# Kernel tuning notes

Measured on AMD Instinct MI355X. Metric: run time of the kernel, lower is better.

The kernel has to match this reference:

```python
import jax, jax.numpy as jnp
import numpy as np

LN_EPS = 1e-5

def _layernorm(x, g, b):
    mu = jnp.mean(x, axis=-1, keepdims=True)
    var = jnp.var(x, axis=-1, keepdims=True)
    return (x - mu) * jax.lax.rsqrt(var + LN_EPS) * g + b

def _attention(q_in, ctx, wq, wk, wv, wo, bo, n_heads):
    b, n, _ = q_in.shape
    m = ctx.shape[1]
    d_attn = wq.shape[1]
    d_head = d_attn // n_heads
    Q = (q_in @ wq).reshape(b, n, n_heads, d_head)
    K = (ctx @ wk).reshape(b, m, n_heads, d_head)
    V = (ctx @ wv).reshape(b, m, n_heads, d_head)
    scale = 1.0 / np.sqrt(d_head).astype(np.float32)
    sim = jnp.einsum('bnhd,bmhd->bhnm', Q, K) * scale
    attn = jax.nn.softmax(sim, axis=-1)
    out = jnp.einsum('bhnm,bmhd->bnhd', attn, V).reshape(b, n, d_attn)
    return out @ wo + bo

def setup_inputs() -> dict:
    key = jax.random.key(0)
    ks = jax.random.split(key, 16)
    B, N, D = 8, 1024, 640
    M, CD = 77, 768
    H = 4 * D  # GEGLU hidden = 2560
    s = lambda d: 1.0 / np.sqrt(d)
    return {
        'x': jax.random.normal(ks[0], (B, N, D), jnp.float32),
        'context': jax.random.normal(ks[1], (B, M, CD), jnp.float32),
        'sa_wq': jax.random.normal(ks[2], (D, D), jnp.float32) * s(D),
        'sa_wk': jax.random.normal(ks[3], (D, D), jnp.float32) * s(D),
        'sa_wv': jax.random.normal(ks[4], (D, D), jnp.float32) * s(D),
        'sa_wo': jax.random.normal(ks[5], (D, D), jnp.float32) * s(D),
        'sa_bo': jnp.zeros((D,), jnp.float32),
        'ca_wq': jax.random.normal(ks[6], (D, D), jnp.float32) * s(D),
        'ca_wk': jax.random.normal(ks[7], (CD, D), jnp.float32) * s(CD),
        'ca_wv': jax.random.normal(ks[8], (CD, D), jnp.float32) * s(CD),
        'ca_wo': jax.random.normal(ks[9], (D, D), jnp.float32) * s(D),
        'ca_bo': jnp.zeros((D,), jnp.float32),
        'ff_w1': jax.random.normal(ks[10], (D, 2 * H), jnp.float32) * s(D),
        'ff_b1': jnp.zeros((2 * H,), jnp.float32),
        'ff_w2': jax.random.normal(ks[11], (H, D), jnp.float32) * s(H),
        'ff_b2': jnp.zeros((D,), jnp.float32),
        'ln1_g': jnp.ones((D,), jnp.float32), 'ln1_b': jnp.zeros((D,), jnp.float32),
        'ln2_g': jnp.ones((D,), jnp.float32), 'ln2_b': jnp.zeros((D,), jnp.float32),
        'ln3_g': jnp.ones((D,), jnp.float32), 'ln3_b': jnp.zeros((D,), jnp.float32),
    }

def reference(x, context, sa_wq, sa_wk, sa_wv, sa_wo, sa_bo,
              ca_wq, ca_wk, ca_wv, ca_wo, ca_bo,
              ff_w1, ff_b1, ff_w2, ff_b2,
              ln1_g, ln1_b, ln2_g, ln2_b, ln3_g, ln3_b):
    n_heads = 8
    # post-norm residual block, matching norm_i(x + sublayer(x))
    x = _layernorm(x + _attention(x, x, sa_wq, sa_wk, sa_wv, sa_wo, sa_bo, n_heads), ln1_g, ln1_b)
    x = _layernorm(x + _attention(x, context, ca_wq, ca_wk, ca_wv, ca_wo, ca_bo, n_heads), ln2_g, ln2_b)
    h = x @ ff_w1 + ff_b1
    a, gate = jnp.split(h, 2, axis=-1)
    ff = (a * jax.nn.gelu(gate, approximate=False)) @ ff_w2 + ff_b2
    x = _layernorm(x + ff, ln3_g, ln3_b)
    return x
```

## Files before the change

### kernel.cpp

```cpp
#include <hip/hip_runtime.h>


using u16 = unsigned short;
typedef __attribute__((ext_vector_type(8))) short bfrag;
typedef __attribute__((ext_vector_type(4))) float f4;
typedef __attribute__((ext_vector_type(4))) unsigned short us4;

#define MFMA(a, b, c) __builtin_amdgcn_mfma_f32_16x16x32_bf16((a), (b), (c), 0, 0, 0)

__device__ __forceinline__ void gload16(const void* g, void* l) {
    __builtin_amdgcn_global_load_lds(
        (const __attribute__((address_space(1))) void*)g,
        (__attribute__((address_space(3))) void*)l, 16, 0, 0);
}

__device__ __forceinline__ u16 f2b(float f) {
    unsigned u = __float_as_uint(f);
    unsigned r = u + 0x7FFFu + ((u >> 16) & 1u);
    return (u16)(r >> 16);
}
__device__ __forceinline__ float b2f(u16 u) {
    return __uint_as_float(((unsigned)u) << 16);
}
__device__ __forceinline__ unsigned pack2(float a, float b) {
    return (unsigned)f2b(a) | ((unsigned)f2b(b) << 16);
}
__device__ __forceinline__ bfrag bzero() {
    bfrag z = {0,0,0,0,0,0,0,0};
    return z;
}
__device__ __forceinline__ float gelu_f(float x) {
    float y = 0.7978845608028654f * (x + 0.044715f * x * x * x);
    float e = exp2f(y * 2.8853900817779268f);
    float t = 1.0f - 2.0f * __builtin_amdgcn_rcpf(e + 1.0f);
    return 0.5f * x * (1.0f + t);
}

__device__ __forceinline__ void transp_tile(const float* __restrict__ in,
                                            u16* __restrict__ out,
                                            int K, int N, int ldo,
                                            int tile, bool perm,
                                            float (*t)[33])
{
    int nw = N >> 5;
    int n0 = (tile % nw) * 32, k0 = (tile / nw) * 32;
    int tx = threadIdx.x & 31, ty = threadIdx.x >> 5;
    #pragma unroll
    for (int i = 0; i < 32; i += 8)
        t[ty + i][tx] = in[(size_t)(k0 + ty + i) * N + n0 + tx];
    __syncthreads();
    #pragma unroll
    for (int i = 0; i < 32; i += 8) {
        int n = n0 + ty + i;
        int dst;
        if (perm) {
            dst = (n < 2560) ? ((n >> 5) * 64 + (n & 31))
                             : (((n - 2560) >> 5) * 64 + 32 + ((n - 2560) & 31));
        } else {
            dst = n;
        }
        out[(size_t)dst * ldo + k0 + tx] = f2b(t[tx][ty + i]);
    }
}

__global__ __launch_bounds__(256) void prep_k(
    const float* __restrict__ x, const float* __restrict__ ctx,
    const float* __restrict__ sa_wq, const float* __restrict__ sa_wk,
    const float* __restrict__ sa_wv, const float* __restrict__ sa_wo,
    const float* __restrict__ ca_wq, const float* __restrict__ ca_wk,
    const float* __restrict__ ca_wv, const float* __restrict__ ca_wo,
    const float* __restrict__ ff_w1, const float* __restrict__ ff_w2,
    u16* saqkvt, u16* sawot, u16* cawqt, u16* cawot, u16* cakvt,
    u16* ffw1t, u16* ffw2t, u16* xb, u16* ctxb)
{
    __shared__ float t[32][33];
    int b = blockIdx.x;
    if (b < 2400) {
        int task = b / 400, tile = b - task * 400;
        const float* src;
        u16* dst;
        if      (task == 0) { src = sa_wq; dst = saqkvt; }
        else if (task == 1) { src = sa_wk; dst = saqkvt + 409600; }
        else if (task == 2) { src = sa_wv; dst = saqkvt + 819200; }
        else if (task == 3) { src = sa_wo; dst = sawot; }
        else if (task == 4) { src = ca_wq; dst = cawqt; }
        else                { src = ca_wo; dst = cawot; }
        transp_tile(src, dst, 640, 640, 640, tile, false, t);
    } else if (b < 3360) {
        int tt = b - 2400;
        int task = tt / 480, tile = tt - task * 480;
        transp_tile(task ? ca_wv : ca_wk, cakvt + task * 491520, 768, 640, 768,
                    tile, false, t);
    } else if (b < 6560) {
        transp_tile(ff_w1, ffw1t, 640, 5120, 640, b - 3360, true, t);
    } else if (b < 8160) {
        transp_tile(ff_w2, ffw2t, 2560, 640, 2560, b - 6560, false, t);
    } else if (b < 10720) {
        int i = (b - 8160) * 256 + threadIdx.x;
        const float4* p = (const float4*)x + (size_t)i * 2;
        float4 a = p[0], bb = p[1];
        uint4 w = { pack2(a.x, a.y), pack2(a.z, a.w),
                    pack2(bb.x, bb.y), pack2(bb.z, bb.w) };
        ((uint4*)xb)[i] = w;
    } else {
        int i = (b - 10720) * 256 + threadIdx.x;
        int rowOut = i / 96, c8 = (i - rowOut * 96) * 8;
        int bb = rowOut / 80, r = rowOut - bb * 80;
        uint4 w = {0, 0, 0, 0};
        if (r < 77) {
            const float4* p = (const float4*)(ctx + ((size_t)(bb * 77 + r)) * 768 + c8);
            float4 a = p[0], b2 = p[1];
            w = (uint4){ pack2(a.x, a.y), pack2(a.z, a.w),
                         pack2(b2.x, b2.y), pack2(b2.z, b2.w) };
        }
        ((uint4*)ctxb)[i] = w;
    }
}

template<int MODE>
__device__ __forceinline__ void gemm_core(const u16* __restrict__ A,
                                          const u16* __restrict__ Bt,
                                          int N, int K,
                                          const float* __restrict__ bias,
                                          const u16* __restrict__ resb,
                                          float* __restrict__ outf,
                                          u16* __restrict__ outb,
                                          u16* __restrict__ out2,
                                          int bx, int by,
                                          u16* As, u16* Bs)
{
    const int lane = threadIdx.x & 63;
    const int wid  = threadIdx.x >> 6;
    const int q    = lane >> 4;
    const int lc   = lane & 15;
    const int wm = wid >> 1, wn = wid & 1;
    const int m0 = by * 128;
    const int n0 = bx * 128;

    f4 acc[4][4];
    #pragma unroll
    for (int i = 0; i < 4; ++i)
        #pragma unroll
        for (int j = 0; j < 4; ++j) acc[i][j] = (f4){0.f, 0.f, 0.f, 0.f};

    const char* Abase = (const char*)A + (size_t)m0 * (size_t)(K * 2);
    const char* Bbase = (const char*)Bt + (size_t)n0 * (size_t)(K * 2);

    for (int kt = 0; kt < K; kt += 64) {
        #pragma unroll
        for (int c = 0; c < 4; ++c) {
            int cid = wid * 4 + c;
            int o = cid * 1024 + lane * 16;
            int row = o >> 7;
            int pc  = o & 127;
            int src = pc ^ ((row & 7) << 4);
            gload16(Abase + (size_t)row * (K * 2) + kt * 2 + src, (char*)As + cid * 1024);
            gload16(Bbase + (size_t)row * (K * 2) + kt * 2 + src, (char*)Bs + cid * 1024);
        }
        __syncthreads();
        #pragma unroll
        for (int ks = 0; ks < 2; ++ks) {
            bfrag a[4], b[4];
            #pragma unroll
            for (int mi = 0; mi < 4; ++mi) {
                int row = wm * 64 + mi * 16 + lc;
                int off = row * 128 + ((ks * 64 + q * 16) ^ ((row & 7) << 4));
                a[mi] = *(const bfrag*)((const char*)As + off);
            }
            #pragma unroll
            for (int ni = 0; ni < 4; ++ni) {
                int row = wn * 64 + ni * 16 + lc;
                int off = row * 128 + ((ks * 64 + q * 16) ^ ((row & 7) << 4));
                b[ni] = *(const bfrag*)((const char*)Bs + off);
            }
            #pragma unroll
            for (int mi = 0; mi < 4; ++mi)
                #pragma unroll
                for (int ni = 0; ni < 4; ++ni)
                    acc[mi][ni] = MFMA(a[mi], b[ni], acc[mi][ni]);
        }
        __syncthreads();
    }

    const int baseRow = m0 + wm * 64;
    const int baseCol = n0 + wn * 64;

    if (MODE == 4) {
        const int blk = baseCol >> 6;
        #pragma unroll
        for (int mi = 0; mi < 4; ++mi)
            #pragma unroll
            for (int ni = 0; ni < 2; ++ni) {
                int j = blk * 32 + ni * 16 + lc;
                float ba = bias[j];
                float bg = bias[2560 + j];
                #pragma unroll
                for (int r = 0; r < 4; ++r) {
                    int row = baseRow + mi * 16 + q * 4 + r;
                    float aa = acc[mi][ni][r] + ba;
                    float gg = acc[mi][ni + 2][r] + bg;
                    outb[(size_t)row * 2560 + j] = f2b(aa * gelu_f(gg));
                }
            }
        return;
    }

    #pragma unroll
    for (int mi = 0; mi < 4; ++mi)
        #pragma unroll
        for (int ni = 0; ni < 4; ++ni) {
            int col = baseCol + ni * 16 + lc;
            if (MODE == 2) {
                const float qs = (col < 640) ? 0.11180339887498949f : 1.0f;
                us4 vv = {0, 0, 0, 0};
                #pragma unroll
                for (int r = 0; r < 4; ++r) {
                    int row = baseRow + mi * 16 + q * 4 + r;
                    u16 u = f2b(acc[mi][ni][r] * qs);
                    outb[(size_t)row * 1920 + col] = u;
                    vv[r] = u;
                }
                if (col >= 1280) {
                    int cd = col - 1280;
                    int hh = cd / 80, dd = cd - hh * 80;
                    int row0 = baseRow + mi * 16 + q * 4;
                    int bb = row0 >> 10, tok = row0 & 1023;
                    *(us4*)&out2[(size_t)((bb * 8 + hh) * 80 + dd) * 1024 + tok] = vv;
                }
            } else {
                #pragma unroll
                for (int r = 0; r < 4; ++r) {
                    int row = baseRow + mi * 16 + q * 4 + r;
                    float v = acc[mi][ni][r];
                    if (MODE == 0) {
                        v += bias[col] + b2f(resb[(size_t)row * N + col]);
                        outf[(size_t)row * N + col] = v;
                    } else if (MODE == 1) {
                        outb[(size_t)row * N + col] = f2b(v);
                    } else if (MODE == 3) {
                        int bb = row / 80, rr = row - bb * 80;
                        if (rr < 77) {
                            u16 u = f2b(v);
                            if (col < 640) {
                                outb[(size_t)row * 640 + col] = u;
                            } else {
                                int cd = col - 640;
                                int hh = cd / 80, dd = cd - hh * 80;
                                out2[((bb * 8 + hh) * 80 + dd) * 80 + rr] = u;
                            }
                        }
                    }
                }
            }
        }
}

template<int MODE>
__global__ __launch_bounds__(256) void gemm_bt(const u16* __restrict__ A,
                                               const u16* __restrict__ Bt,
                                               int N, int K,
                                               const float* __restrict__ bias,
                                               const u16* __restrict__ resb,
                                               float* __restrict__ outf,
                                               u16* __restrict__ outb,
                                               u16* __restrict__ out2)
{
    __shared__ u16 As[128 * 64];
    __shared__ u16 Bs[128 * 64];
    gemm_core<MODE>(A, Bt, N, K, bias, resb, outf, outb, out2,
                    blockIdx.x, blockIdx.y, As, Bs);
}

__global__ __launch_bounds__(256) void gemm_qkv_cakv(
    const u16* __restrict__ xb, const u16* __restrict__ saqkvt,
    const u16* __restrict__ ctxb, const u16* __restrict__ cakvt,
    u16* qkvb, u16* vt, u16* kc, u16* vct)
{
    __shared__ u16 As[128 * 64];
    __shared__ u16 Bs[128 * 64];
    int bid = blockIdx.x;
    if (bid < 960) {
        gemm_core<2>(xb, saqkvt, 1920, 640, nullptr, nullptr, nullptr,
                     qkvb, vt, bid % 15, bid / 15, As, Bs);
    } else {
        int tt = bid - 960;
        gemm_core<3>(ctxb, cakvt, 1280, 768, nullptr, nullptr, nullptr,
                     kc, vct, tt % 10, tt / 10, As, Bs);
    }
}

__global__ __launch_bounds__(256) void attn_sa(const u16* __restrict__ qkv,
                                               const u16* __restrict__ vt,
                                               u16* __restrict__ out)
{
    __shared__ u16 Qs[64 * 80];
    __shared__ u16 Ks[64 * 80];
    __shared__ u16 Vs[80 * 64];
    __shared__ u16 Ps[4][16 * 64];

    const int lane = threadIdx.x & 63;
    const int wid  = threadIdx.x >> 6;
    const int hi   = lane >> 4;
    const int lc   = lane & 15;
    const int bid = blockIdx.x;
    const int qt = bid >> 6;
    const int bb = (bid >> 3) & 7;
    const int hh = bid & 7;
    const int tok0 = bb * 1024 + qt * 64;
    const char* qbase = (const char*)qkv;

    for (int c = wid; c < 10; c += 4) {
        int o = c * 1024 + lane * 16;
        int row = o / 160, col = o - row * 160;
        gload16(qbase + (size_t)(tok0 + row) * 3840 + hh * 160 + col, (char*)Qs + c * 1024);
    }
    __syncthreads();

    const int qrow = wid * 16 + lc;
    bfrag qf0 = *(const bfrag*)((const char*)Qs + qrow * 160 + hi * 16);
    bfrag qf1 = *(const bfrag*)((const char*)Qs + qrow * 160 + 64 + hi * 16);
    bfrag qf2 = bzero();
    if (hi < 2) qf2 = *(const bfrag*)((const char*)Qs + qrow * 160 + 128 + hi * 16);

    float m = -3e30f, l = 0.f;
    f4 accO[5];
    #pragma unroll
    for (int no = 0; no < 5; ++no) accO[no] = (f4){0.f, 0.f, 0.f, 0.f};

    const float L2E = 1.4426950408889634f;

    for (int t = 0; t < 16; ++t) {
        __syncthreads();
        for (int c = wid; c < 20; c += 4) {
            if (c < 10) {
                int o = c * 1024 + lane * 16;
                int row = o / 160, col = o - row * 160;
                gload16(qbase + (size_t)(bb * 1024 + t * 64 + row) * 3840 + 1280 + hh * 160 + col,
                        (char*)Ks + c * 1024);
            } else {
                int c2 = c - 10;
                int o = c2 * 1024 + lane * 16;
                int row = o >> 7;
                int pc  = o & 127;
                int src = pc ^ ((row & 7) << 4);
                gload16((const char*)vt + (size_t)((bb * 8 + hh) * 80 + row) * 2048 + t * 128 + src,
                        (char*)Vs + c2 * 1024);
            }
        }
        __syncthreads();

        f4 sT[4];
        #pragma unroll
        for (int nb = 0; nb < 4; ++nb) {
            const char* kb = (const char*)Ks + (nb * 16 + lc) * 160;
            bfrag k0 = *(const bfrag*)(kb + hi * 16);
            bfrag k1 = *(const bfrag*)(kb + 64 + hi * 16);
            bfrag k2 = bzero();
            if (hi < 2) k2 = *(const bfrag*)(kb + 128 + hi * 16);
            f4 a = {0.f, 0.f, 0.f, 0.f};
            a = MFMA(k0, qf0, a);
            a = MFMA(k1, qf1, a);
            a = MFMA(k2, qf2, a);
            sT[nb] = a;
        }

        float pm = sT[0][0];
        #pragma unroll
        for (int nb = 0; nb < 4; ++nb)
            #pragma unroll
            for (int r = 0; r < 4; ++r) pm = fmaxf(pm, sT[nb][r]);
        pm = fmaxf(pm, __shfl_xor(pm, 16));
        pm = fmaxf(pm, __shfl_xor(pm, 32));

        if (__any(pm > m + 8.0f)) {
            float mn = fmaxf(m, pm);
            float al = exp2f((m - mn) * L2E);
            m = mn;
            l *= al;
            float af[4];
            #pragma unroll
            for (int r = 0; r < 4; ++r) af[r] = __shfl(al, hi * 4 + r);
            #pragma unroll
            for (int no = 0; no < 5; ++no)
                #pragma unroll
                for (int r = 0; r < 4; ++r) accO[no][r] *= af[r];
        }

        float sum = 0.f;
        #pragma unroll
        for (int nb = 0; nb < 4; ++nb)
            #pragma unroll
            for (int r = 0; r < 4; ++r) {
                float p = exp2f((sT[nb][r] - m) * L2E);
                sT[nb][r] = p;
                sum += p;
            }
        sum += __shfl_xor(sum, 16);
        sum += __shfl_xor(sum, 32);
        l += sum;

        char* Pw = (char*)&Ps[wid][0];
        #pragma unroll
        for (int nb = 0; nb < 4; ++nb) {
            us4 pk = { f2b(sT[nb][0]), f2b(sT[nb][1]), f2b(sT[nb][2]), f2b(sT[nb][3]) };
            int cb = (nb * 16 + hi * 4) * 2;
            *(us4*)(Pw + lc * 128 + (cb ^ ((lc & 7) << 4))) = pk;
        }

        bfrag pa0 = *(const bfrag*)(Pw + lc * 128 + ((hi * 16) ^ ((lc & 7) << 4)));
        bfrag pa1 = *(const bfrag*)(Pw + lc * 128 + ((64 + hi * 16) ^ ((lc & 7) << 4)));
        #pragma unroll
        for (int no = 0; no < 5; ++no) {
            int vr = no * 16 + lc;
            const char* vb = (const char*)Vs + vr * 128;
            bfrag v0 = *(const bfrag*)(vb + ((hi * 16) ^ ((vr & 7) << 4)));
            bfrag v1 = *(const bfrag*)(vb + ((64 + hi * 16) ^ ((vr & 7) << 4)));
            accO[no] = MFMA(pa0, v0, accO[no]);
            accO[no] = MFMA(pa1, v1, accO[no]);
        }
    }

    float rf[4];
    #pragma unroll
    for (int r = 0; r < 4; ++r) {
        float lf = __shfl(l, hi * 4 + r);
        rf[r] = __builtin_amdgcn_rcpf(lf);
    }
    #pragma unroll
    for (int no = 0; no < 5; ++no)
        #pragma unroll
        for (int r = 0; r < 4; ++r) {
            int row = tok0 + wid * 16 + hi * 4 + r;
            int col = hh * 80 + no * 16 + lc;
            out[(size_t)row * 640 + col] = f2b(accO[no][r] * rf[r]);
        }
}

__global__ __launch_bounds__(256) void attn_ca(const u16* __restrict__ qc,
                                               const u16* __restrict__ kc,
                                               const u16* __restrict__ vct,
                                               u16* __restrict__ out)
{
    __shared__ u16 Qs[64 * 80];
    __shared__ u16 Ks[84 * 80];
    __shared__ u16 Vs[84 * 80];
    __shared__ u16 Ps[4][16 * 80];

    const int lane = threadIdx.x & 63;
    const int wid  = threadIdx.x >> 6;
    const int q    = lane >> 4;
    const int lc   = lane & 15;
    const int bid = blockIdx.x;
    const int qt = bid & 15;
    const int hh = (bid >> 4) & 7;
    const int bb = bid >> 7;
    const int tok0 = bb * 1024 + qt * 64;

    for (int c = wid; c < 36; c += 4) {
        if (c < 10) {
            int o = c * 1024 + lane * 16;
            int row = o / 160, col = o - row * 160;
            gload16((const char*)qc + (size_t)(tok0 + row) * 1280 + hh * 160 + col,
                    (char*)Qs + c * 1024);
        } else if (c < 23) {
            int c2 = c - 10;
            int o = c2 * 1024 + lane * 16;
            int row = o / 160, col = o - row * 160;
            gload16((const char*)kc + (size_t)(bb * 80 + row) * 1280 + hh * 160 + col,
                    (char*)Ks + c2 * 1024);
        } else {
            int c2 = c - 23;
            int o = c2 * 1024 + lane * 16;
            int row = o / 160, col = o - row * 160;
            gload16((const char*)vct + (size_t)((bb * 8 + hh) * 80 + row) * 160 + col,
                    (char*)Vs + c2 * 1024);
        }
    }
    __syncthreads();

    const int qrow = wid * 16 + lc;
    bfrag qf0 = *(const bfrag*)((const char*)Qs + qrow * 160 + q * 16);
    bfrag qf1 = *(const bfrag*)((const char*)Qs + qrow * 160 + 64 + q * 16);
    bfrag qf2 = bzero();
    if (q < 2) qf2 = *(const bfrag*)((const char*)Qs + qrow * 160 + 128 + q * 16);

    const float SC = 0.11180339887498949f;
    const float L2E = 1.4426950408889634f;

    f4 s[5];
    #pragma unroll
    for (int nb = 0; nb < 5; ++nb) {
        const char* kb = (const char*)Ks + (nb * 16 + lc) * 160;
        bfrag k0 = *(const bfrag*)(kb + q * 16);
        bfrag k1 = *(const bfrag*)(kb + 64 + q * 16);
        bfrag k2 = bzero();
        if (q < 2) k2 = *(const bfrag*)(kb + 128 + q * 16);
        f4 a = {0.f, 0.f, 0.f, 0.f};
        a = MFMA(qf0, k0, a);
        a = MFMA(qf1, k1, a);
        a = MFMA(qf2, k2, a);
        s[nb] = a;
    }
    #pragma unroll
    for (int nb = 0; nb < 5; ++nb) {
        int key = nb * 16 + lc;
        #pragma unroll
        for (int r = 0; r < 4; ++r) {
            s[nb][r] *= SC;
            if (key >= 77) s[nb][r] = -1e30f;
        }
    }
    float mrow[4], lrow[4];
    #pragma unroll
    for (int r = 0; r < 4; ++r) {
        float v = fmaxf(fmaxf(fmaxf(s[0][r], s[1][r]), fmaxf(s[2][r], s[3][r])), s[4][r]);
        v = fmaxf(v, __shfl_xor(v, 1));
        v = fmaxf(v, __shfl_xor(v, 2));
        v = fmaxf(v, __shfl_xor(v, 4));
        v = fmaxf(v, __shfl_xor(v, 8));
        mrow[r] = v;
    }
    float rsum[4] = {0.f, 0.f, 0.f, 0.f};
    #pragma unroll
    for (int nb = 0; nb < 5; ++nb)
        #pragma unroll
        for (int r = 0; r < 4; ++r) {
            float p = exp2f((s[nb][r] - mrow[r]) * L2E);
            s[nb][r] = p;
            rsum[r] += p;
        }
    #pragma unroll
    for (int r = 0; r < 4; ++r) {
        float v = rsum[r];
        v += __shfl_xor(v, 1);
        v += __shfl_xor(v, 2);
        v += __shfl_xor(v, 4);
        v += __shfl_xor(v, 8);
        lrow[r] = v;
    }

    char* Pw = (char*)&Ps[wid][0];
    #pragma unroll
    for (int nb = 0; nb < 5; ++nb)
        #pragma unroll
        for (int r = 0; r < 4; ++r) {
            int prow = q * 4 + r;
            *(u16*)(Pw + prow * 160 + (nb * 16 + lc) * 2) = f2b(s[nb][r]);
        }
    bfrag pa0 = *(const bfrag*)(Pw + lc * 160 + q * 16);
    bfrag pa1 = *(const bfrag*)(Pw + lc * 160 + 64 + q * 16);
    bfrag pa2 = bzero();
    if (q < 2) pa2 = *(const bfrag*)(Pw + lc * 160 + 128 + q * 16);

    f4 accO[5];
    #pragma unroll
    for (int no = 0; no < 5; ++no) {
        const char* vb = (const char*)Vs + (no * 16 + lc) * 160;
        bfrag v0 = *(const bfrag*)(vb + q * 16);
        bfrag v1 = *(const bfrag*)(vb + 64 + q * 16);
        bfrag v2 = bzero();
        if (q < 2) v2 = *(const bfrag*)(vb + 128 + q * 16);
        f4 a = {0.f, 0.f, 0.f, 0.f};
        a = MFMA(pa0, v0, a);
        a = MFMA(pa1, v1, a);
        a = MFMA(pa2, v2, a);
        accO[no] = a;
    }
    #pragma unroll
    for (int no = 0; no < 5; ++no)
        #pragma unroll
        for (int r = 0; r < 4; ++r) {
            int row = tok0 + wid * 16 + q * 4 + r;
            int col = hh * 80 + no * 16 + lc;
            out[(size_t)row * 640 + col] = f2b(accO[no][r] / lrow[r]);
        }
}

__global__ __launch_bounds__(256) void ln_k(const float* __restrict__ pre,
                                            const float* __restrict__ g,
                                            const float* __restrict__ b,
                                            float* __restrict__ xo,
                                            u16* __restrict__ xb)
{
    const int lane = threadIdx.x & 63;
    const int wid  = threadIdx.x >> 6;
    const int row = blockIdx.x * 4 + wid;
    const float* p = pre + (size_t)row * 640;
    float v[10];
    #pragma unroll
    for (int i = 0; i < 10; ++i) v[i] = p[lane + i * 64];
    float s = 0.f;
    #pragma unroll
    for (int i = 0; i < 10; ++i) s += v[i];
    #pragma unroll
    for (int m = 1; m < 64; m <<= 1) s += __shfl_xor(s, m);
    float mu = s * (1.0f / 640.0f);
    float d2 = 0.f;
    #pragma unroll
    for (int i = 0; i < 10; ++i) { float d = v[i] - mu; d2 += d * d; }
    #pragma unroll
    for (int m = 1; m < 64; m <<= 1) d2 += __shfl_xor(d2, m);
    float rs = rsqrtf(d2 * (1.0f / 640.0f) + 1e-5f);
    #pragma unroll
    for (int i = 0; i < 10; ++i) {
        int col = lane + i * 64;
        float y = (v[i] - mu) * rs * g[col] + b[col];
        if (xo) xo[(size_t)row * 640 + col] = y;
        if (xb) xb[(size_t)row * 640 + col] = f2b(y);
    }
}

extern "C" void kernel_launch(void* const* d_in, const int* in_sizes, int n_in,
                              void* d_out, int out_size, void* d_ws, size_t ws_size,
                              hipStream_t stream)
{
    const float* x       = (const float*)d_in[0];
    const float* context = (const float*)d_in[1];
    const float* sa_wq = (const float*)d_in[2];
    const float* sa_wk = (const float*)d_in[3];
    const float* sa_wv = (const float*)d_in[4];
    const float* sa_wo = (const float*)d_in[5];
    const float* sa_bo = (const float*)d_in[6];
    const float* ca_wq = (const float*)d_in[7];
    const float* ca_wk = (const float*)d_in[8];
    const float* ca_wv = (const float*)d_in[9];
    const float* ca_wo = (const float*)d_in[10];
    const float* ca_bo = (const float*)d_in[11];
    const float* ff_w1 = (const float*)d_in[12];
    const float* ff_b1 = (const float*)d_in[13];
    const float* ff_w2 = (const float*)d_in[14];
    const float* ff_b2 = (const float*)d_in[15];
    const float* ln1_g = (const float*)d_in[16];
    const float* ln1_b = (const float*)d_in[17];
    const float* ln2_g = (const float*)d_in[18];
    const float* ln2_b = (const float*)d_in[19];
    const float* ln3_g = (const float*)d_in[20];
    const float* ln3_b = (const float*)d_in[21];

    char* ws = (char*)d_ws;
    const size_t OFF_XB     = 0;
    const size_t OFF_QKVB   = 10485760;
    const size_t OFF_VT     = 41943040;
    const size_t OFF_AB     = 52428800;
    const size_t OFF_ATTN   = 62914560;
    const size_t OFF_QC     = 73400320;
    const size_t OFF_KC     = 83886080;
    const size_t OFF_VCT    = 84705280;
    const size_t OFF_SAQKVT = 85524480;
    const size_t OFF_SAWOT  = 87982080;
    const size_t OFF_CAWQT  = 88801280;
    const size_t OFF_CAKVT  = 89620480;
    const size_t OFF_CAWOT  = 91586560;
    const size_t OFF_FFW1T  = 92405760;
    const size_t OFF_FFW2T  = 98959360;
    const size_t OFF_CTXB   = 102236160;
    const size_t OFF_PRE    = 103219200;

    u16* xb      = (u16*)(ws + OFF_XB);
    u16* qkvb    = (u16*)(ws + OFF_QKVB);
    u16* vt      = (u16*)(ws + OFF_VT);
    u16* ab      = (u16*)(ws + OFF_AB);
    u16* attnb   = (u16*)(ws + OFF_ATTN);
    u16* qc      = (u16*)(ws + OFF_QC);
    u16* kc      = (u16*)(ws + OFF_KC);
    u16* vct     = (u16*)(ws + OFF_VCT);
    u16* saqkvt  = (u16*)(ws + OFF_SAQKVT);
    u16* sawot   = (u16*)(ws + OFF_SAWOT);
    u16* cawqt   = (u16*)(ws + OFF_CAWQT);
    u16* cakvt   = (u16*)(ws + OFF_CAKVT);
    u16* cawot   = (u16*)(ws + OFF_CAWOT);
    u16* ffw1t   = (u16*)(ws + OFF_FFW1T);
    u16* ffw2t   = (u16*)(ws + OFF_FFW2T);
    u16* ctxb    = (u16*)(ws + OFF_CTXB);
    float* pre   = (float*)(ws + OFF_PRE);
    u16* ffh     = (u16*)(ws + OFF_XB);

    hipLaunchKernelGGL(prep_k, dim3(10960), dim3(256), 0, stream,
                       x, context, sa_wq, sa_wk, sa_wv, sa_wo, ca_wq, ca_wk,
                       ca_wv, ca_wo, ff_w1, ff_w2,
                       saqkvt, sawot, cawqt, cawot, cakvt, ffw1t, ffw2t, xb, ctxb);

    hipLaunchKernelGGL(gemm_qkv_cakv, dim3(1010), dim3(256), 0, stream,
                       xb, saqkvt, ctxb, cakvt, qkvb, vt, kc, vct);
    hipLaunchKernelGGL(attn_sa, dim3(1024), dim3(256), 0, stream, qkvb, vt, attnb);
    hipLaunchKernelGGL(gemm_bt<0>, dim3(5, 64), dim3(256), 0, stream,
                       attnb, sawot, 640, 640, sa_bo, xb, pre,
                       (u16*)nullptr, (u16*)nullptr);
    hipLaunchKernelGGL(ln_k, dim3(2048), dim3(256), 0, stream, pre, ln1_g, ln1_b,
                       (float*)nullptr, ab);

    hipLaunchKernelGGL(gemm_bt<1>, dim3(5, 64), dim3(256), 0, stream,
                       ab, cawqt, 640, 640, (const float*)nullptr, (const u16*)nullptr,
                       (float*)nullptr, qc, (u16*)nullptr);
    hipLaunchKernelGGL(attn_ca, dim3(1024), dim3(256), 0, stream, qc, kc, vct, attnb);
    hipLaunchKernelGGL(gemm_bt<0>, dim3(5, 64), dim3(256), 0, stream,
                       attnb, cawot, 640, 640, ca_bo, ab, pre,
                       (u16*)nullptr, (u16*)nullptr);
    hipLaunchKernelGGL(ln_k, dim3(2048), dim3(256), 0, stream, pre, ln2_g, ln2_b,
                       (float*)nullptr, ab);

    hipLaunchKernelGGL(gemm_bt<4>, dim3(40, 64), dim3(256), 0, stream,
                       ab, ffw1t, 5120, 640, ff_b1, (const u16*)nullptr,
                       (float*)nullptr, ffh, (u16*)nullptr);
    hipLaunchKernelGGL(gemm_bt<0>, dim3(5, 64), dim3(256), 0, stream,
                       ffh, ffw2t, 640, 2560, ff_b2, ab, pre,
                       (u16*)nullptr, (u16*)nullptr);
    hipLaunchKernelGGL(ln_k, dim3(2048), dim3(256), 0, stream, pre, ln3_g, ln3_b,
                       (float*)d_out, (u16*)nullptr);
}
```

Measured before the change: 355.3 us.

## Add dedicated 256x256 double-buffered FF1 GEMM kernel with fused GEGLU epilogue

```diff
diff --git a/kernel.cpp b/kernel.cpp
--- a/kernel.cpp
+++ b/kernel.cpp
@@ -184,26 +184,6 @@
 
     const int baseRow = m0 + wm * 64;
     const int baseCol = n0 + wn * 64;
-
-    if (MODE == 4) {
-        const int blk = baseCol >> 6;
-        #pragma unroll
-        for (int mi = 0; mi < 4; ++mi)
-            #pragma unroll
-            for (int ni = 0; ni < 2; ++ni) {
-                int j = blk * 32 + ni * 16 + lc;
-                float ba = bias[j];
-                float bg = bias[2560 + j];
-                #pragma unroll
-                for (int r = 0; r < 4; ++r) {
-                    int row = baseRow + mi * 16 + q * 4 + r;
-                    float aa = acc[mi][ni][r] + ba;
-                    float gg = acc[mi][ni + 2][r] + bg;
-                    outb[(size_t)row * 2560 + j] = f2b(aa * gelu_f(gg));
-                }
-            }
-        return;
-    }
 
     #pragma unroll
     for (int mi = 0; mi < 4; ++mi)
@@ -289,6 +269,133 @@
     }
 }
 
+__device__ __forceinline__ void stage_kt(const char* Ab, const char* Bb,
+                                         char* buf, int jb, int tid)
+{
+    #pragma unroll
+    for (int h = 0; h < 2; ++h) {
+        #pragma unroll
+        for (int s = 0; s < 2; ++s) {
+            int o = s * 8192 + tid * 16;
+            int row = o >> 7;
+            int src = (o & 127) ^ ((row & 7) << 4);
+            gload16(Ab + (size_t)(h * 128 + row) * 1280 + jb + src,
+                    buf + h * 16384 + o);
+            gload16(Bb + (size_t)(h * 128 + row) * 1280 + jb + src,
+                    buf + 32768 + h * 16384 + o);
+        }
+    }
+}
+
+__global__ __launch_bounds__(512, 2) void gemm_ff1(const u16* __restrict__ A,
+                                                   const u16* __restrict__ Bt,
+                                                   const float* __restrict__ bias,
+                                                   u16* __restrict__ outb)
+{
+    __shared__ __attribute__((aligned(16))) char lds[131072];
+    const int tid = threadIdx.x;
+    const int lane = tid & 63;
+    const int wid = tid >> 6;
+    const int hi = lane >> 4;
+    const int lc = lane & 15;
+    const int wm = wid >> 2;
+    const int wn = wid & 3;
+    int wg = (blockIdx.x & 7) * 80 + (blockIdx.x >> 3);
+    const int by = wg / 20, bx = wg - (wg / 20) * 20;
+    const int m0 = by * 256, n0 = bx * 256;
+
+    const char* Ab = (const char*)A + (size_t)m0 * 1280;
+    const char* Bb = (const char*)Bt + (size_t)n0 * 1280;
+
+    f4 acc[8][4];
+    #pragma unroll
+    for (int i = 0; i < 8; ++i)
+        #pragma unroll
+        for (int j = 0; j < 4; ++j) acc[i][j] = (f4){0.f, 0.f, 0.f, 0.f};
+
+    const int swz = (lc & 7) << 4;
+    const char* Ards = lds + wm * 16384;
+    const char* Brds = lds + 32768 + (wn >> 1) * 16384;
+    const int brow0 = (wn & 1) * 64;
+
+    stage_kt(Ab, Bb, lds, 0, tid);
+    asm volatile("s_waitcnt vmcnt(0)" ::: "memory");
+    __builtin_amdgcn_sched_barrier(0);
+    asm volatile("s_barrier" ::: "memory");
+
+    #pragma unroll 1
+    for (int i = 0; i < 5; ++i) {
+        #pragma unroll
+        for (int kk = 0; kk < 2; ++kk) {
+            const char* Ak = Ards + kk * 65536;
+            const char* Bk = Brds + kk * 65536;
+            bfrag bfr[4][2];
+            #pragma unroll
+            for (int qd = 0; qd < 4; ++qd) {
+                if (qd == 0) {
+                    #pragma unroll
+                    for (int ni = 0; ni < 4; ++ni)
+                        #pragma unroll
+                        for (int ks = 0; ks < 2; ++ks)
+                            bfr[ni][ks] = *(const bfrag*)(Bk
+                                + (brow0 + ni * 16 + lc) * 128
+                                + ((ks * 64 + hi * 16) ^ swz));
+                }
+                bfrag a0[2], a1[2];
+                #pragma unroll
+                for (int ks = 0; ks < 2; ++ks) {
+                    a0[ks] = *(const bfrag*)(Ak + ((2 * qd) * 16 + lc) * 128
+                                 + ((ks * 64 + hi * 16) ^ swz));
+                    a1[ks] = *(const bfrag*)(Ak + ((2 * qd + 1) * 16 + lc) * 128
+                                 + ((ks * 64 + hi * 16) ^ swz));
+                }
+                if (qd == 0) {
+                    if (kk == 0) {
+                        stage_kt(Ab, Bb, lds + 65536, (2 * i + 1) * 128, tid);
+                    } else if (i < 4) {
+                        stage_kt(Ab, Bb, lds, (2 * i + 2) * 128, tid);
+                    }
+                }
+                __builtin_amdgcn_sched_barrier(0);
+                asm volatile("s_barrier" ::: "memory");
+                asm volatile("s_waitcnt lgkmcnt(0)" ::: "memory");
+                __builtin_amdgcn_sched_barrier(0);
+                __builtin_amdgcn_s_setprio(1);
+                #pragma unroll
+                for (int ni = 0; ni < 4; ++ni) {
+                    acc[2 * qd][ni]     = MFMA(a0[0], bfr[ni][0], acc[2 * qd][ni]);
+                    acc[2 * qd][ni]     = MFMA(a0[1], bfr[ni][1], acc[2 * qd][ni]);
+                    acc[2 * qd + 1][ni] = MFMA(a1[0], bfr[ni][0], acc[2 * qd + 1][ni]);
+                    acc[2 * qd + 1][ni] = MFMA(a1[1], bfr[ni][1], acc[2 * qd + 1][ni]);
+                }
+                __builtin_amdgcn_s_setprio(0);
+                if (qd == 3)
+                    asm volatile("s_waitcnt vmcnt(0)" ::: "memory");
+                __builtin_amdgcn_sched_barrier(0);
+                asm volatile("s_barrier" ::: "memory");
+            }
+        }
+    }
+
+    const int baseRow = m0 + wm * 128;
+    const int blk = (n0 + wn * 64) >> 6;
+    #pragma unroll
+    for (int mi = 0; mi < 8; ++mi)
+        #pragma unroll
+        for (int ni = 0; ni < 2; ++ni) {
+            int j = blk * 32 + ni * 16 + lc;
+            float ba = bias[j];
+            float bg = bias[2560 + j];
+            #pragma unroll
+            for (int r = 0; r < 4; ++r) {
+                int row = baseRow + mi * 16 + hi * 4 + r;
+                float aa = acc[mi][ni][r] + ba;
+                float gg = acc[mi][ni + 2][r] + bg;
+                outb[(size_t)row * 2560 + j] = f2b(aa * gelu_f(gg));
+            }
+        }
+}
+
 __global__ __launch_bounds__(256) void attn_sa(const u16* __restrict__ qkv,
                                                const u16* __restrict__ vt,
                                                u16* __restrict__ out)
@@ -699,9 +806,8 @@
     hipLaunchKernelGGL(ln_k, dim3(2048), dim3(256), 0, stream, pre, ln2_g, ln2_b,
                        (float*)nullptr, ab);
 
-    hipLaunchKernelGGL(gemm_bt<4>, dim3(40, 64), dim3(256), 0, stream,
-                       ab, ffw1t, 5120, 640, ff_b1, (const u16*)nullptr,
-                       (float*)nullptr, ffh, (u16*)nullptr);
+    hipLaunchKernelGGL(gemm_ff1, dim3(640), dim3(512), 0, stream,
+                       ab, ffw1t, ff_b1, ffh);
     hipLaunchKernelGGL(gemm_bt<0>, dim3(5, 64), dim3(256), 0, stream,
                        ffh, ffw2t, 640, 2560, ff_b2, ab, pre,
                        (u16*)nullptr, (u16*)nullptr);
```

After: 361.0 us. About the same (+1.6%).

## Split FF2 GEMM along K into two halves and sum partials in layernorm

Applied to the files above, without the earlier changes.

```diff
diff --git a/kernel.cpp b/kernel.cpp
--- a/kernel.cpp
+++ b/kernel.cpp
@@ -120,7 +120,7 @@
 template<int MODE>
 __device__ __forceinline__ void gemm_core(const u16* __restrict__ A,
                                           const u16* __restrict__ Bt,
-                                          int N, int K,
+                                          int N, int K, int ld,
                                           const float* __restrict__ bias,
                                           const u16* __restrict__ resb,
                                           float* __restrict__ outf,
@@ -136,6 +136,7 @@
     const int wm = wid >> 1, wn = wid & 1;
     const int m0 = by * 128;
     const int n0 = bx * 128;
+    const int ldb = ld * 2;
 
     f4 acc[4][4];
     #pragma unroll
@@ -143,8 +144,8 @@
         #pragma unroll
         for (int j = 0; j < 4; ++j) acc[i][j] = (f4){0.f, 0.f, 0.f, 0.f};
 
-    const char* Abase = (const char*)A + (size_t)m0 * (size_t)(K * 2);
-    const char* Bbase = (const char*)Bt + (size_t)n0 * (size_t)(K * 2);
+    const char* Abase = (const char*)A + (size_t)m0 * ldb;
+    const char* Bbase = (const char*)Bt + (size_t)n0 * ldb;
 
     for (int kt = 0; kt < K; kt += 64) {
         #pragma unroll
@@ -154,8 +155,8 @@
             int row = o >> 7;
             int pc  = o & 127;
             int src = pc ^ ((row & 7) << 4);
-            gload16(Abase + (size_t)row * (K * 2) + kt * 2 + src, (char*)As + cid * 1024);
-            gload16(Bbase + (size_t)row * (K * 2) + kt * 2 + src, (char*)Bs + cid * 1024);
+            gload16(Abase + (size_t)row * ldb + kt * 2 + src, (char*)As + cid * 1024);
+            gload16(Bbase + (size_t)row * ldb + kt * 2 + src, (char*)Bs + cid * 1024);
         }
         __syncthreads();
         #pragma unroll
@@ -235,6 +236,8 @@
                     if (MODE == 0) {
                         v += bias[col] + b2f(resb[(size_t)row * N + col]);
                         outf[(size_t)row * N + col] = v;
+                    } else if (MODE == 6) {
+                        outf[(size_t)row * N + col] = v;
                     } else if (MODE == 1) {
                         outb[(size_t)row * N + col] = f2b(v);
                     } else if (MODE == 3) {
@@ -267,7 +270,7 @@
 {
     __shared__ u16 As[128 * 64];
     __shared__ u16 Bs[128 * 64];
-    gemm_core<MODE>(A, Bt, N, K, bias, resb, outf, outb, out2,
+    gemm_core<MODE>(A, Bt, N, K, K, bias, resb, outf, outb, out2,
                     blockIdx.x, blockIdx.y, As, Bs);
 }
 
@@ -280,12 +283,31 @@
     __shared__ u16 Bs[128 * 64];
     int bid = blockIdx.x;
     if (bid < 960) {
-        gemm_core<2>(xb, saqkvt, 1920, 640, nullptr, nullptr, nullptr,
+        gemm_core<2>(xb, saqkvt, 1920, 640, 640, nullptr, nullptr, nullptr,
                      qkvb, vt, bid % 15, bid / 15, As, Bs);
     } else {
         int tt = bid - 960;
-        gemm_core<3>(ctxb, cakvt, 1280, 768, nullptr, nullptr, nullptr,
+        gemm_core<3>(ctxb, cakvt, 1280, 768, 768, nullptr, nullptr, nullptr,
                      kc, vct, tt % 10, tt / 10, As, Bs);
+    }
+}
+
+__global__ __launch_bounds__(256) void gemm_ff2(const u16* __restrict__ ffh,
+                                                const u16* __restrict__ ffw2t,
+                                                const float* __restrict__ bias,
+                                                const u16* __restrict__ resb,
+                                                float* preA, float* preB)
+{
+    __shared__ u16 As[128 * 64];
+    __shared__ u16 Bs[128 * 64];
+    int bid = blockIdx.x;
+    if (bid < 320) {
+        gemm_core<0>(ffh, ffw2t, 640, 1280, 2560, bias, resb, preA,
+                     nullptr, nullptr, bid % 5, bid / 5, As, Bs);
+    } else {
+        bid -= 320;
+        gemm_core<6>(ffh + 1280, ffw2t + 1280, 640, 1280, 2560, nullptr, nullptr,
+                     preB, nullptr, nullptr, bid % 5, bid / 5, As, Bs);
     }
 }
 
@@ -607,6 +629,39 @@
         float y = (v[i] - mu) * rs * g[col] + b[col];
         if (xo) xo[(size_t)row * 640 + col] = y;
         if (xb) xb[(size_t)row * 640 + col] = f2b(y);
+    }
+}
+
+__global__ __launch_bounds__(256) void ln_k2(const float* __restrict__ preA,
+                                             const float* __restrict__ preB,
+                                             const float* __restrict__ g,
+                                             const float* __restrict__ b,
+                                             float* __restrict__ xo)
+{
+    const int lane = threadIdx.x & 63;
+    const int wid  = threadIdx.x >> 6;
+    const int row = blockIdx.x * 4 + wid;
+    const float* pa = preA + (size_t)row * 640;
+    const float* pb = preB + (size_t)row * 640;
+    float v[10];
+    #pragma unroll
+    for (int i = 0; i < 10; ++i) v[i] = pa[lane + i * 64] + pb[lane + i * 64];
+    float s = 0.f;
+    #pragma unroll
+    for (int i = 0; i < 10; ++i) s += v[i];
+    #pragma unroll
+    for (int m = 1; m < 64; m <<= 1) s += __shfl_xor(s, m);
+    float mu = s * (1.0f / 640.0f);
+    float d2 = 0.f;
+    #pragma unroll
+    for (int i = 0; i < 10; ++i) { float d = v[i] - mu; d2 += d * d; }
+    #pragma unroll
+    for (int m = 1; m < 64; m <<= 1) d2 += __shfl_xor(d2, m);
+    float rs = rsqrtf(d2 * (1.0f / 640.0f) + 1e-5f);
+    #pragma unroll
+    for (int i = 0; i < 10; ++i) {
+        int col = lane + i * 64;
+        xo[(size_t)row * 640 + col] = (v[i] - mu) * rs * g[col] + b[col];
     }
 }
 
@@ -655,6 +710,7 @@
     const size_t OFF_FFW2T  = 98959360;
     const size_t OFF_CTXB   = 102236160;
     const size_t OFF_PRE    = 103219200;
+    const size_t OFF_PREB   = 124190720;
 
     u16* xb      = (u16*)(ws + OFF_XB);
     u16* qkvb    = (u16*)(ws + OFF_QKVB);
@@ -673,6 +729,7 @@
     u16* ffw2t   = (u16*)(ws + OFF_FFW2T);
     u16* ctxb    = (u16*)(ws + OFF_CTXB);
     float* pre   = (float*)(ws + OFF_PRE);
+    float* preB  = (float*)(ws + OFF_PREB);
     u16* ffh     = (u16*)(ws + OFF_XB);
 
     hipLaunchKernelGGL(prep_k, dim3(10960), dim3(256), 0, stream,
@@ -702,9 +759,8 @@
     hipLaunchKernelGGL(gemm_bt<4>, dim3(40, 64), dim3(256), 0, stream,
                        ab, ffw1t, 5120, 640, ff_b1, (const u16*)nullptr,
                        (float*)nullptr, ffh, (u16*)nullptr);
-    hipLaunchKernelGGL(gemm_bt<0>, dim3(5, 64), dim3(256), 0, stream,
-                       ffh, ffw2t, 640, 2560, ff_b2, ab, pre,
-                       (u16*)nullptr, (u16*)nullptr);
-    hipLaunchKernelGGL(ln_k, dim3(2048), dim3(256), 0, stream, pre, ln3_g, ln3_b,
-                       (float*)d_out, (u16*)nullptr);
-}
+    hipLaunchKernelGGL(gemm_ff2, dim3(640), dim3(256), 0, stream,
+                       ffh, ffw2t, ff_b2, ab, pre, preB);
+    hipLaunchKernelGGL(ln_k2, dim3(2048), dim3(256), 0, stream, pre, preB,
+                       ln3_g, ln3_b, (float*)d_out);
+}
```

New measurement: 359.1 us. No clear change (+1.1%).
